# Performance work log

Hardware: AMD Instinct MI355X
Metric: run time of the kernel (lower is better)

## Reference

```python
import jax, jax.numpy as jnp
import numpy as np

DIM = 4096
N_HEADS = 32
N_KV_HEADS = 8
HEAD_DIM = 128
N_REP = N_HEADS // N_KV_HEADS  # 4
Q_DIM = N_HEADS * HEAD_DIM     # 4096
K_DIM = N_KV_HEADS * HEAD_DIM  # 1024
B, T = 2, 2048
ROPE_THETA = 10000.0


def setup_inputs() -> dict:
    key = jax.random.key(0)
    k1, k2, k3, k4 = jax.random.split(key, 4)
    x = jax.random.normal(k1, (B, T, DIM), dtype=jnp.float32)
    wqkv = jax.random.normal(k2, (Q_DIM + 2 * K_DIM, DIM), dtype=jnp.float32) * 0.02
    wo = jax.random.normal(k3, (DIM, DIM), dtype=jnp.float32) * 0.02
    # RoPE tables: [max_T, head_dim//2]
    inv_freq = 1.0 / (ROPE_THETA ** (jnp.arange(0, HEAD_DIM, 2, dtype=jnp.float32) / HEAD_DIM))
    angles = jnp.arange(T, dtype=jnp.float32)[:, None] * inv_freq[None, :]  # [T, D/2]
    cos = jnp.cos(angles)
    sin = jnp.sin(angles)
    freqs_cis = jax.random.normal(k4, (T, HEAD_DIM // 2), dtype=jnp.float32)  # unused by forward
    return {"x": x, "freqs_cis": freqs_cis, "wqkv": wqkv, "wo": wo, "cos": cos, "sin": sin}


def _apply_rope(q, k, cos, sin):
    # q: [B,T,Hq,D], k: [B,T,Hkv,D]; interleaved even/odd pairs
    Tlen = q.shape[1]
    c = cos[:Tlen][None, :, None, :]  # [1,T,1,D/2]
    s = sin[:Tlen][None, :, None, :]

    def rot(t):
        tr, ti = t[..., 0::2], t[..., 1::2]
        or_ = tr * c - ti * s
        oi = tr * s + ti * c
        return jnp.stack([or_, oi], axis=-1).reshape(t.shape)

    return rot(q), rot(k)


def reference(x, freqs_cis, wqkv, wo, cos, sin):
    Bx, Tx, _ = x.shape
    qkv = jnp.einsum('btd,ed->bte', x, wqkv)  # fused QKV GEMM
    q = qkv[..., :Q_DIM].reshape(Bx, Tx, N_HEADS, HEAD_DIM)
    k = qkv[..., Q_DIM:Q_DIM + K_DIM].reshape(Bx, Tx, N_KV_HEADS, HEAD_DIM)
    v = qkv[..., Q_DIM + K_DIM:].reshape(Bx, Tx, N_KV_HEADS, HEAD_DIM)
    q, k = _apply_rope(q, k, cos, sin)
    # GQA repeat_interleave over head dim
    k = jnp.repeat(k, N_REP, axis=2)  # [B,T,Hq,D]
    v = jnp.repeat(v, N_REP, axis=2)
    scale = 1.0 / jnp.sqrt(jnp.asarray(HEAD_DIM, dtype=q.dtype))
    scores = jnp.einsum('bqhd,bkhd->bhqk', q, k) * scale  # [B,H,T,T]
    causal = jnp.tril(jnp.ones((Tx, Tx), dtype=bool))
    scores = jnp.where(causal[None, None], scores, jnp.finfo(scores.dtype).min)
    probs = jax.nn.softmax(scores, axis=-1)
    y = jnp.einsum('bhqk,bkhd->bqhd', probs, v).reshape(Bx, Tx, Q_DIM)
    return jnp.einsum('btd,ed->bte', y, wo)
```

## Files before the change

kernel.cpp:

```cpp
#include <hip/hip_runtime.h>

#define T_SEQ 2048
#define NB    2
#define NH    32
#define NKV   8
#define HD    128
#define DIM   4096
#define EDIM  6144
#define M_TOK 4096

typedef __bf16          bf8  __attribute__((ext_vector_type(8)));
typedef unsigned short  us8  __attribute__((ext_vector_type(8)));
typedef float           f4   __attribute__((ext_vector_type(4)));
typedef float           f16v __attribute__((ext_vector_type(16)));
typedef int             i4   __attribute__((ext_vector_type(4)));

__device__ inline unsigned short f2bf(float f) {
  unsigned int u = __builtin_bit_cast(unsigned int, f);
  u += 0x7FFF + ((u >> 16) & 1);
  return (unsigned short)(u >> 16);
}
__device__ inline float bf2f(unsigned short h) {
  unsigned int u = ((unsigned int)h) << 16;
  return __builtin_bit_cast(float, u);
}
__device__ inline void gl_lds16(const void* g, void* l) {
  __builtin_amdgcn_global_load_lds(
      (const __attribute__((address_space(1))) unsigned int*)g,
      (__attribute__((address_space(3))) unsigned int*)l, 16, 0, 0);
}
__device__ inline f4 mfma16(bf8 a, bf8 b, f4 c) {
  return __builtin_amdgcn_mfma_f32_16x16x32_bf16(a, b, c, 0, 0, 0);
}
__device__ inline f16v mfma32(bf8 a, bf8 b, f16v c) {
  return __builtin_amdgcn_mfma_f32_32x32x16_bf16(a, b, c, 0, 0, 0);
}
__device__ inline unsigned cvtpk(float lo, float hi) {
  unsigned r;
  asm("v_cvt_pk_bf16_f32 %0, %1, %2" : "=v"(r) : "v"(lo), "v"(hi));
  return r;
}

__global__ void k_f2bf3(const float* __restrict__ x, const float* __restrict__ wq,
                        const float* __restrict__ wo,
                        unsigned short* __restrict__ xb, unsigned short* __restrict__ wqb,
                        unsigned short* __restrict__ wob) {
  const long n0 = (long)M_TOK * DIM / 4;
  const long n1 = (long)EDIM * DIM / 4;
  const long n2 = (long)DIM * DIM / 4;
  const long total = n0 + n1 + n2;
  const long stride = (long)gridDim.x * blockDim.x;
  for (long i = (long)blockIdx.x * blockDim.x + threadIdx.x; i < total; i += stride) {
    const float* in; unsigned short* out; long j = i;
    if (j < n0)              { in = x;  out = xb; }
    else if ((j -= n0) < n1) { in = wq; out = wqb; }
    else       { j -= n1;      in = wo; out = wob; }
    f4 v = *(const f4*)(in + j * 4);
    unsigned long long pack =
        (unsigned long long)f2bf(v[0]) |
        ((unsigned long long)f2bf(v[1]) << 16) |
        ((unsigned long long)f2bf(v[2]) << 32) |
        ((unsigned long long)f2bf(v[3]) << 48);
    *(unsigned long long*)(out + j * 4) = pack;
  }
}

__global__ __launch_bounds__(512, 2)
void k_gemm384(const unsigned short* __restrict__ A, const unsigned short* __restrict__ Bm,
               unsigned short* __restrict__ oQ, unsigned short* __restrict__ oK,
               unsigned short* __restrict__ oV) {
  __shared__ unsigned short As[2][8192];
  __shared__ unsigned short Bs[2][3][8192];
  const int n0 = blockIdx.x;
  const int x = n0 & 7, ix = n0 >> 3;
  const int bm = ((x >> 1) << 3) + (ix >> 3);
  const int bn = ((x & 1) << 3) + (ix & 7);
  const int t = threadIdx.x;
  const int lane = t & 63, w = t >> 6;
  const int wr = w >> 2, wc = w & 3;
  const int l15 = lane & 15, lhi = lane >> 4;
  const int KT = DIM >> 6;

  f4 acc[4][6] = {};

  const int tt0 = t * 8;
  auto stA = [&](int buf, int tile) {
    if (tile >= KT) return;
    const unsigned short* gp = A + (size_t)(bm * 128) * DIM + tile * 64;
#pragma unroll
    for (int j = 0; j < 2; ++j) {
      int e = j * 4096 + tt0;
      int rl = e >> 6, cs = (e & 63) ^ ((rl & 7) << 3);
      gl_lds16(gp + (size_t)rl * DIM + cs, &As[buf][e]);
    }
  };
  auto stB = [&](int buf, int bh, int tile) {
    if (tile >= KT) return;
    const unsigned short* gp = Bm + (size_t)(bn * 384 + bh * 128) * DIM + tile * 64;
#pragma unroll
    for (int j = 0; j < 2; ++j) {
      int e = j * 4096 + tt0;
      int rl = e >> 6, cs = (e & 63) ^ ((rl & 7) << 3);
      gl_lds16(gp + (size_t)rl * DIM + cs, &Bs[buf][bh][e]);
    }
  };
  auto rdA = [&](int buf, int mi, int kk) -> bf8 {
    int row = wr * 64 + mi * 16 + l15;
    int col = (lhi * 8 + kk * 32) ^ ((row & 7) << 3);
    return __builtin_bit_cast(bf8, *(const us8*)&As[buf][row * 64 + col]);
  };
  auto rdB = [&](int buf, int bh, int ni, int kk) -> bf8 {
    int row = wc * 32 + ni * 16 + l15;
    int col = (lhi * 8 + kk * 32) ^ ((row & 7) << 3);
    return __builtin_bit_cast(bf8, *(const us8*)&Bs[buf][bh][row * 64 + col]);
  };
  auto bar = [&]() {
    asm volatile("" ::: "memory");
    __builtin_amdgcn_s_barrier();
    asm volatile("" ::: "memory");
  };
  auto lgkm0 = [&]() {
    asm volatile("s_waitcnt lgkmcnt(0)" ::: "memory");
    __builtin_amdgcn_sched_barrier(0);
  };

  stA(0, 0); stB(0, 0, 0); stB(0, 1, 0); stB(0, 2, 0);
  asm volatile("s_waitcnt vmcnt(4)" ::: "memory");
  bar();

  for (int tp = 0; tp < KT; tp += 2) {
#pragma unroll
    for (int sub = 0; sub < 2; ++sub) {
      const int tc = tp + sub, b = sub;
      const bool last = (tc == KT - 1);
      bf8 af[4][2], bfr[2][2];
#pragma unroll
      for (int mi = 0; mi < 4; ++mi)
#pragma unroll
        for (int kk = 0; kk < 2; ++kk) af[mi][kk] = rdA(b, mi, kk);
#pragma unroll
      for (int ni = 0; ni < 2; ++ni)
#pragma unroll
        for (int kk = 0; kk < 2; ++kk) bfr[ni][kk] = rdB(b, 0, ni, kk);
      stA(b ^ 1, tc + 1); stB(b ^ 1, 0, tc + 1);
      lgkm0();
      __builtin_amdgcn_s_setprio(1);
#pragma unroll
      for (int mi = 0; mi < 4; ++mi)
#pragma unroll
        for (int ni = 0; ni < 2; ++ni)
#pragma unroll
          for (int kk = 0; kk < 2; ++kk)
            acc[mi][ni] = mfma16(af[mi][kk], bfr[ni][kk], acc[mi][ni]);
      __builtin_amdgcn_s_setprio(0);
      if (last) { asm volatile("s_waitcnt vmcnt(2)" ::: "memory"); }
      else      { asm volatile("s_waitcnt vmcnt(6)" ::: "memory"); }
      bar();
#pragma unroll
      for (int ni = 0; ni < 2; ++ni)
#pragma unroll
        for (int kk = 0; kk < 2; ++kk) bfr[ni][kk] = rdB(b, 1, ni, kk);
      stB(b ^ 1, 1, tc + 1);
      lgkm0();
      __builtin_amdgcn_s_setprio(1);
#pragma unroll
      for (int mi = 0; mi < 4; ++mi)
#pragma unroll
        for (int ni = 0; ni < 2; ++ni)
#pragma unroll
          for (int kk = 0; kk < 2; ++kk)
            acc[mi][2 + ni] = mfma16(af[mi][kk], bfr[ni][kk], acc[mi][2 + ni]);
      __builtin_amdgcn_s_setprio(0);
      if (last) { asm volatile("s_waitcnt vmcnt(0)" ::: "memory"); }
      else      { asm volatile("s_waitcnt vmcnt(6)" ::: "memory"); }
      bar();
#pragma unroll
      for (int ni = 0; ni < 2; ++ni)
#pragma unroll
        for (int kk = 0; kk < 2; ++kk) bfr[ni][kk] = rdB(b, 2, ni, kk);
      stB(b ^ 1, 2, tc + 1);
      lgkm0();
      __builtin_amdgcn_s_setprio(1);
#pragma unroll
      for (int mi = 0; mi < 4; ++mi)
#pragma unroll
        for (int ni = 0; ni < 2; ++ni)
#pragma unroll
          for (int kk = 0; kk < 2; ++kk)
            acc[mi][4 + ni] = mfma16(af[mi][kk], bfr[ni][kk], acc[mi][4 + ni]);
      __builtin_amdgcn_s_setprio(0);
      if (!last) { asm volatile("s_waitcnt vmcnt(4)" ::: "memory"); }
      bar();
    }
  }

#pragma unroll
  for (int bh = 0; bh < 3; ++bh)
#pragma unroll
    for (int ni = 0; ni < 2; ++ni) {
      const int colb = bn * 384 + bh * 128 + wc * 32 + ni * 16;
      unsigned short* op; int ldo, c0;
      if (colb < 4096)      { op = oQ; ldo = 4096; c0 = colb; }
      else if (colb < 5120) { op = oK; ldo = 1024; c0 = colb - 4096; }
      else                  { op = oV; ldo = 1024; c0 = colb - 5120; }
#pragma unroll
      for (int mi = 0; mi < 4; ++mi)
#pragma unroll
        for (int rr = 0; rr < 4; ++rr) {
          int row = bm * 128 + wr * 64 + mi * 16 + lhi * 4 + rr;
          op[(size_t)row * ldo + c0 + l15] = f2bf(acc[mi][bh * 2 + ni][rr]);
        }
    }
}

#define MFMA_Q(a0, b0, AF, BF)                                        \
  __builtin_amdgcn_s_setprio(1);                                      \
  _Pragma("unroll") for (int mi = 0; mi < 4; ++mi)                    \
  _Pragma("unroll") for (int ni = 0; ni < 2; ++ni)                    \
  _Pragma("unroll") for (int kk = 0; kk < 2; ++kk)                    \
      acc[(a0) + mi][(b0) + ni] =                                     \
          mfma16(AF[mi][kk], BF[ni][kk], acc[(a0) + mi][(b0) + ni]);  \
  __builtin_amdgcn_s_setprio(0);

#define RD_A(buf, mh)                                                 \
  _Pragma("unroll") for (int mi = 0; mi < 4; ++mi)                    \
  _Pragma("unroll") for (int kk = 0; kk < 2; ++kk)                    \
      af[mi][kk] = rdA(buf, mh, mi, kk);

#define RD_B(buf, nh, BF)                                             \
  _Pragma("unroll") for (int ni = 0; ni < 2; ++ni)                    \
  _Pragma("unroll") for (int kk = 0; kk < 2; ++kk)                    \
      BF[ni][kk] = rdB(buf, nh, ni, kk);

__global__ __launch_bounds__(512, 2)
void k_gemm256f(const unsigned short* __restrict__ A, const unsigned short* __restrict__ Bm,
                float* __restrict__ oF) {
  __shared__ unsigned short As[2][16384];
  __shared__ unsigned short Bs[2][16384];
  const int n0 = blockIdx.x;
  const int x = n0 & 7, ix = n0 >> 3;
  const int bm = ((x >> 1) << 2) + (ix >> 3);
  const int bn = ((x & 1) << 3) + (ix & 7);
  const int N = DIM, K = DIM;
  const int t = threadIdx.x;
  const int lane = t & 63, w = t >> 6;
  const int wr = w >> 2, wc = w & 3;
  const int l15 = lane & 15, lhi = lane >> 4;
  const int KT = K >> 6;
  const int NI = KT >> 1;

  f4 acc[8][4] = {};

  const int tt0 = t * 8;
  auto stA = [&](int buf, int half, int tile) {
    if (tile >= KT) return;
    const unsigned short* gp = A + (size_t)(bm * 256 + half * 128) * K + tile * 64;
#pragma unroll
    for (int j = 0; j < 2; ++j) {
      int e = j * 4096 + tt0;
      int rl = e >> 6;
      int cs = (e & 63) ^ ((rl & 7) << 3);
      gl_lds16(gp + (size_t)rl * K + cs, &As[buf][half * 8192 + e]);
    }
  };
  auto stB = [&](int buf, int half, int tile) {
    if (tile >= KT) return;
    const unsigned short* gp = Bm + (size_t)(bn * 256 + half * 128) * K + tile * 64;
#pragma unroll
    for (int j = 0; j < 2; ++j) {
      int e = j * 4096 + tt0;
      int rl = e >> 6;
      int cs = (e & 63) ^ ((rl & 7) << 3);
      gl_lds16(gp + (size_t)rl * K + cs, &Bs[buf][half * 8192 + e]);
    }
  };
  auto rdA = [&](int buf, int mh, int mi, int kk) -> bf8 {
    int row = mh * 128 + wr * 64 + mi * 16 + l15;
    int col = (lhi * 8 + kk * 32) ^ ((row & 7) << 3);
    return __builtin_bit_cast(bf8, *(const us8*)&As[buf][row * 64 + col]);
  };
  auto rdB = [&](int buf, int nh, int ni, int kk) -> bf8 {
    int row = nh * 128 + wc * 32 + ni * 16 + l15;
    int col = (lhi * 8 + kk * 32) ^ ((row & 7) << 3);
    return __builtin_bit_cast(bf8, *(const us8*)&Bs[buf][row * 64 + col]);
  };
  auto bar = [&]() {
    asm volatile("" ::: "memory");
    __builtin_amdgcn_s_barrier();
    asm volatile("" ::: "memory");
  };
  auto lgkm0 = [&]() {
    asm volatile("s_waitcnt lgkmcnt(0)" ::: "memory");
    __builtin_amdgcn_sched_barrier(0);
  };

  stA(0, 0, 0); stB(0, 1, 0); stA(0, 1, 0); stB(0, 0, 0);
  stA(1, 0, 1); stB(1, 1, 1); stA(1, 1, 1);
  asm volatile("s_waitcnt vmcnt(6)" ::: "memory");
  bar();

  for (int i = 0; i < NI; ++i) {
    const int t2 = 2 * i + 2, t3 = 2 * i + 3;
    bf8 af[4][2], bf0[2][2], bf1[2][2];
    RD_A(0, 0); RD_B(0, 0, bf0);
    stB(1, 0, 2 * i + 1);
    lgkm0();
    MFMA_Q(0, 0, af, bf0);
    bar();
    RD_B(0, 1, bf1);
    stA(0, 0, t2);
    lgkm0();
    MFMA_Q(0, 2, af, bf1);
    bar();
    RD_A(0, 1);
    stB(0, 1, t2);
    lgkm0();
    MFMA_Q(4, 2, af, bf1);
    bar();
    stA(0, 1, t2);
    MFMA_Q(4, 0, af, bf0);
    if (i + 1 < NI) { asm volatile("s_waitcnt vmcnt(6)" ::: "memory"); }
    else            { asm volatile("s_waitcnt vmcnt(0)" ::: "memory"); }
    bar();
    RD_A(1, 0); RD_B(1, 0, bf0);
    stB(0, 0, t2);
    lgkm0();
    MFMA_Q(0, 0, af, bf0);
    bar();
    RD_B(1, 1, bf1);
    stA(1, 0, t3);
    lgkm0();
    MFMA_Q(0, 2, af, bf1);
    bar();
    RD_A(1, 1);
    stB(1, 1, t3);
    lgkm0();
    MFMA_Q(4, 2, af, bf1);
    bar();
    stA(1, 1, t3);
    MFMA_Q(4, 0, af, bf0);
    if (i + 1 < NI) { asm volatile("s_waitcnt vmcnt(6)" ::: "memory"); }
    bar();
  }

  const int rb0 = bm * 256 + wr * 64 + lhi * 4;
  const int cb0 = bn * 256 + wc * 32 + l15;
#pragma unroll
  for (int ai = 0; ai < 8; ++ai)
#pragma unroll
    for (int bj = 0; bj < 4; ++bj)
#pragma unroll
      for (int rr = 0; rr < 4; ++rr) {
        int row = rb0 + (ai >> 2) * 128 + (ai & 3) * 16 + rr;
        int col = cb0 + (bj >> 1) * 128 + (bj & 1) * 16;
        oF[(size_t)row * N + col] = acc[ai][bj][rr];
      }
}

__global__ __launch_bounds__(512, 2)
void k_attn(const unsigned short* __restrict__ Qb, const unsigned short* __restrict__ Kb,
            const unsigned short* __restrict__ Vb, unsigned short* __restrict__ Yb,
            const float* __restrict__ cosp, const float* __restrict__ sinp) {
  __shared__ unsigned short Ks[64 * 128];
  __shared__ unsigned short Vt[128 * 64];
  const int idx = blockIdx.x;
  const int p = idx >> 6;
  const int hb = idx & 63;
  const int h = hb >> 1;
  const int b = hb & 1;
  const int kvh = h >> 2;
  const int t = threadIdx.x;
  const int lane = t & 63, w = t >> 6;
  const int l31 = lane & 31, hh = lane >> 5;
  const float BNEG = -1.0e30f;
  const float QSCALE = (float)(0.08838834764831845 * 1.4426950408889634);
  const int swz = (l31 & 7) << 3;
  const int krow = t >> 4;
  const int kcol = (t & 15) * 8;

  for (int qq = 0; qq < 2; ++qq) {
    const int qblk = qq ? p : 7 - p;
    const int qb0 = qblk * 256;
    const int NT = (qblk + 1) * 4;
    const int wqmin = qb0 + w * 32;
    const int q_g = wqmin + l31;

    bf8 qf[8];
    {
      const unsigned short* qp = Qb + (size_t)(b * T_SEQ + q_g) * 4096 + h * 128 + hh * 8;
#pragma unroll
      for (int st = 0; st < 8; ++st) {
        us8 v = *(const us8*)(qp + st * 16);
        f4 c = *(const f4*)(cosp + q_g * 64 + st * 8 + hh * 4);
        f4 s = *(const f4*)(sinp + q_g * 64 + st * 8 + hh * 4);
        us8 o;
#pragma unroll
        for (int j = 0; j < 4; ++j) {
          float tr = bf2f(v[2 * j]), ti = bf2f(v[2 * j + 1]);
          o[2 * j]     = f2bf((tr * c[j] - ti * s[j]) * QSCALE);
          o[2 * j + 1] = f2bf((tr * s[j] + ti * c[j]) * QSCALE);
        }
        qf[st] = __builtin_bit_cast(bf8, o);
      }
    }
    float m_run = BNEG, l_run = 0.f;
    f16v yacc[4] = {};

    for (int kt = 0; kt < NT; ++kt) {
      const int kbase = kt * 64;
      const unsigned short* vp = Vb + (size_t)(b * T_SEQ + kbase + lane) * 1024 + kvh * 128 + w * 8;
      us8 vv0 = *(const us8*)vp;
      us8 vv1 = *(const us8*)(vp + 64);
      const unsigned short* kp = Kb + (size_t)(b * T_SEQ + kbase + krow) * 1024 + kvh * 128 + kcol;
      us8 kk0 = *(const us8*)kp;
      us8 kk1 = *(const us8*)(kp + (size_t)32 * 1024);
      f4 kc0 = *(const f4*)(cosp + (kbase + krow) * 64 + (kcol >> 1));
      f4 ks0 = *(const f4*)(sinp + (kbase + krow) * 64 + (kcol >> 1));
      f4 kc1 = *(const f4*)(cosp + (kbase + krow + 32) * 64 + (kcol >> 1));
      f4 ks1 = *(const f4*)(sinp + (kbase + krow + 32) * 64 + (kcol >> 1));
      __syncthreads();
      {
        us8 o0, o1;
#pragma unroll
        for (int j = 0; j < 4; ++j) {
          float tr0 = bf2f(kk0[2 * j]), ti0 = bf2f(kk0[2 * j + 1]);
          o0[2 * j]     = f2bf(tr0 * kc0[j] - ti0 * ks0[j]);
          o0[2 * j + 1] = f2bf(tr0 * ks0[j] + ti0 * kc0[j]);
          float tr1 = bf2f(kk1[2 * j]), ti1 = bf2f(kk1[2 * j + 1]);
          o1[2 * j]     = f2bf(tr1 * kc1[j] - ti1 * ks1[j]);
          o1[2 * j + 1] = f2bf(tr1 * ks1[j] + ti1 * kc1[j]);
        }
        *(us8*)&Ks[krow * 128 + (kcol ^ ((krow & 7) << 3))] = o0;
        *(us8*)&Ks[(krow + 32) * 128 + (kcol ^ ((krow & 7) << 3))] = o1;
      }
#pragma unroll
      for (int j = 0; j < 8; ++j) {
        int d0 = w * 8 + j;
        Vt[(d0 * 64 + lane) ^ ((d0 & 7) << 3)] = vv0[j];
        int d1 = d0 + 64;
        Vt[(d1 * 64 + lane) ^ ((d1 & 7) << 3)] = vv1[j];
      }
      __syncthreads();
      if (kbase > wqmin + 31) continue;

      f16v s0 = {}, s1 = {};
#pragma unroll
      for (int st = 0; st < 8; ++st) {
        int coff = st * 16 + hh * 8;
        bf8 a0 = __builtin_bit_cast(bf8, *(const us8*)&Ks[(l31 * 128 + coff) ^ swz]);
        bf8 a1 = __builtin_bit_cast(bf8, *(const us8*)&Ks[((l31 + 32) * 128 + coff) ^ swz]);
        s0 = mfma32(a0, qf[st], s0);
        s1 = mfma32(a1, qf[st], s1);
      }
      if (kbase + 63 > wqmin) {
#pragma unroll
        for (int r = 0; r < 16; ++r) {
          int kv = kbase + (r & 3) + 8 * (r >> 2) + 4 * hh;
          if (kv > q_g)      s0[r] = BNEG;
          if (kv + 32 > q_g) s1[r] = BNEG;
        }
      }
      float tmax = BNEG;
#pragma unroll
      for (int r = 0; r < 16; ++r) {
        tmax = fmaxf(tmax, s0[r]);
        tmax = fmaxf(tmax, s1[r]);
      }
      tmax = fmaxf(tmax, __shfl_xor(tmax, 32));
      float m_new = fmaxf(m_run, tmax);
      float fac = exp2f(m_run - m_new);
      m_run = m_new;
      float psum = 0.f;
#pragma unroll
      for (int r = 0; r < 16; ++r) {
        s0[r] = exp2f(s0[r] - m_new); psum += s0[r];
        s1[r] = exp2f(s1[r] - m_new); psum += s1[r];
      }
      psum += __shfl_xor(psum, 32);
      l_run = l_run * fac + psum;
      if (!__all(fac == 1.0f)) {
        float facr[16];
#pragma unroll
        for (int r = 0; r < 16; ++r)
          facr[r] = __shfl(fac, (r & 3) + 8 * (r >> 2) + 4 * hh);
#pragma unroll
        for (int dc = 0; dc < 4; ++dc)
#pragma unroll
          for (int r = 0; r < 16; ++r) yacc[dc][r] *= facr[r];
      }
#pragma unroll
      for (int st = 0; st < 4; ++st) {
        f16v sv = (st & 2) ? s1 : s0;
        const int rb = (st & 1) * 8;
        unsigned pkA = cvtpk(sv[rb + 0], sv[rb + 1]);
        unsigned pkB = cvtpk(sv[rb + 2], sv[rb + 3]);
        unsigned pkC = cvtpk(sv[rb + 4], sv[rb + 5]);
        unsigned pkD = cvtpk(sv[rb + 6], sv[rb + 7]);
        unsigned xA = __shfl_xor(pkA, 32);
        unsigned xB = __shfl_xor(pkB, 32);
        unsigned xC = __shfl_xor(pkC, 32);
        unsigned xD = __shfl_xor(pkD, 32);
        unsigned w0 = hh ? xC : pkA;
        unsigned w1 = hh ? xD : pkB;
        unsigned w2 = hh ? pkC : xA;
        unsigned w3 = hh ? pkD : xB;
        i4 wi = { (int)w0, (int)w1, (int)w2, (int)w3 };
        bf8 pf = __builtin_bit_cast(bf8, wi);
#pragma unroll
        for (int dc = 0; dc < 4; ++dc) {
          int d = dc * 32 + l31;
          bf8 vf = __builtin_bit_cast(bf8, *(const us8*)&Vt[(d * 64 + st * 16 + hh * 8) ^ swz]);
          yacc[dc] = mfma32(pf, vf, yacc[dc]);
        }
      }
    }
    float inv_l = 1.0f / l_run;
    float il[16];
#pragma unroll
    for (int r = 0; r < 16; ++r)
      il[r] = __shfl(inv_l, (r & 3) + 8 * (r >> 2) + 4 * hh);
#pragma unroll
    for (int dc = 0; dc < 4; ++dc)
#pragma unroll
      for (int r = 0; r < 16; ++r) {
        int qrow = qb0 + w * 32 + (r & 3) + 8 * (r >> 2) + 4 * hh;
        Yb[(size_t)(b * T_SEQ + qrow) * 4096 + h * 128 + dc * 32 + l31] =
            f2bf(yacc[dc][r] * il[r]);
      }
  }
}

extern "C" void kernel_launch(void* const* d_in, const int* in_sizes, int n_in,
                              void* d_out, int out_size, void* d_ws, size_t ws_size,
                              hipStream_t stream) {
  const float* x    = (const float*)d_in[0];
  const float* wqkv = (const float*)d_in[2];
  const float* wo   = (const float*)d_in[3];
  const float* cosp = (const float*)d_in[4];
  const float* sinp = (const float*)d_in[5];
  float* out = (float*)d_out;

  char* ws = (char*)d_ws;
  size_t o = 0;
  auto alloc = [&](size_t bytes) { void* p = ws + o; o += (bytes + 255) & ~(size_t)255; return p; };
  unsigned short* x_b    = (unsigned short*)alloc((size_t)M_TOK * DIM * 2);
  unsigned short* wqkv_b = (unsigned short*)alloc((size_t)EDIM * DIM * 2);
  unsigned short* wo_b   = (unsigned short*)alloc((size_t)DIM * DIM * 2);
  unsigned short* Qb     = (unsigned short*)alloc((size_t)M_TOK * 4096 * 2);
  unsigned short* Kb     = (unsigned short*)alloc((size_t)M_TOK * 1024 * 2);
  unsigned short* Vb     = (unsigned short*)alloc((size_t)M_TOK * 1024 * 2);
  unsigned short* Yb     = (unsigned short*)alloc((size_t)M_TOK * 4096 * 2);
  if (o > ws_size) return;

  k_f2bf3<<<2048, 256, 0, stream>>>(x, wqkv, wo, x_b, wqkv_b, wo_b);

  k_gemm384<<<dim3(512), 512, 0, stream>>>(x_b, wqkv_b, Qb, Kb, Vb);

  k_attn<<<dim3(256, 1, 1), 512, 0, stream>>>(Qb, Kb, Vb, Yb, cosp, sinp);

  k_gemm256f<<<dim3(256), 512, 0, stream>>>(Yb, wo_b, out);
}
```

Before: 512.9 us.

## Single-buffer QKV GEMM LDS to raise occupancy to four blocks per CU

Replaces the double-buffered A/B LDS tiles (128KB) of the fused QKV GEMM with a single buffer (64KB) and raises the launch bound to four 512-thread blocks per CU. The loads for the next K tile are issued piecewise into sub-tiles as soon as each is consumed, with barriers and vmcnt waits reworked. This trades intra-block prefetch depth for more resident waves to hide latency. It risks exposing global load latency and register pressure from the tighter launch bound, which could spill the 24 accumulators.

```diff
diff --git a/kernel.cpp b/kernel.cpp
--- a/kernel.cpp
+++ b/kernel.cpp
@@ -65,12 +65,12 @@
   }
 }
 
-__global__ __launch_bounds__(512, 2)
+__global__ __launch_bounds__(512, 4)
 void k_gemm384(const unsigned short* __restrict__ A, const unsigned short* __restrict__ Bm,
                unsigned short* __restrict__ oQ, unsigned short* __restrict__ oK,
                unsigned short* __restrict__ oV) {
-  __shared__ unsigned short As[2][8192];
-  __shared__ unsigned short Bs[2][3][8192];
+  __shared__ unsigned short As[8192];
+  __shared__ unsigned short Bs[3][8192];
   const int n0 = blockIdx.x;
   const int x = n0 & 7, ix = n0 >> 3;
   const int bm = ((x >> 1) << 3) + (ix >> 3);
@@ -84,35 +84,35 @@
   f4 acc[4][6] = {};
 
   const int tt0 = t * 8;
-  auto stA = [&](int buf, int tile) {
+  auto stA = [&](int tile) {
     if (tile >= KT) return;
     const unsigned short* gp = A + (size_t)(bm * 128) * DIM + tile * 64;
 #pragma unroll
     for (int j = 0; j < 2; ++j) {
       int e = j * 4096 + tt0;
       int rl = e >> 6, cs = (e & 63) ^ ((rl & 7) << 3);
-      gl_lds16(gp + (size_t)rl * DIM + cs, &As[buf][e]);
-    }
-  };
-  auto stB = [&](int buf, int bh, int tile) {
+      gl_lds16(gp + (size_t)rl * DIM + cs, &As[e]);
+    }
+  };
+  auto stB = [&](int bh, int tile) {
     if (tile >= KT) return;
     const unsigned short* gp = Bm + (size_t)(bn * 384 + bh * 128) * DIM + tile * 64;
 #pragma unroll
     for (int j = 0; j < 2; ++j) {
       int e = j * 4096 + tt0;
       int rl = e >> 6, cs = (e & 63) ^ ((rl & 7) << 3);
-      gl_lds16(gp + (size_t)rl * DIM + cs, &Bs[buf][bh][e]);
-    }
-  };
-  auto rdA = [&](int buf, int mi, int kk) -> bf8 {
+      gl_lds16(gp + (size_t)rl * DIM + cs, &Bs[bh][e]);
+    }
+  };
+  auto rdA = [&](int mi, int kk) -> bf8 {
     int row = wr * 64 + mi * 16 + l15;
     int col = (lhi * 8 + kk * 32) ^ ((row & 7) << 3);
-    return __builtin_bit_cast(bf8, *(const us8*)&As[buf][row * 64 + col]);
-  };
-  auto rdB = [&](int buf, int bh, int ni, int kk) -> bf8 {
+    return __builtin_bit_cast(bf8, *(const us8*)&As[row * 64 + col]);
+  };
+  auto rdB = [&](int bh, int ni, int kk) -> bf8 {
     int row = wc * 32 + ni * 16 + l15;
     int col = (lhi * 8 + kk * 32) ^ ((row & 7) << 3);
-    return __builtin_bit_cast(bf8, *(const us8*)&Bs[buf][bh][row * 64 + col]);
+    return __builtin_bit_cast(bf8, *(const us8*)&Bs[bh][row * 64 + col]);
   };
   auto bar = [&]() {
     asm volatile("" ::: "memory");
@@ -124,72 +124,69 @@
     __builtin_amdgcn_sched_barrier(0);
   };
 
-  stA(0, 0); stB(0, 0, 0); stB(0, 1, 0); stB(0, 2, 0);
-  asm volatile("s_waitcnt vmcnt(4)" ::: "memory");
+  stA(0); stB(0, 0); stB(1, 0);
+  asm volatile("s_waitcnt vmcnt(2)" ::: "memory");
   bar();
 
-  for (int tp = 0; tp < KT; tp += 2) {
-#pragma unroll
-    for (int sub = 0; sub < 2; ++sub) {
-      const int tc = tp + sub, b = sub;
-      const bool last = (tc == KT - 1);
-      bf8 af[4][2], bfr[2][2];
-#pragma unroll
-      for (int mi = 0; mi < 4; ++mi)
-#pragma unroll
-        for (int kk = 0; kk < 2; ++kk) af[mi][kk] = rdA(b, mi, kk);
+  for (int tc = 0; tc < KT; ++tc) {
+    const bool last = (tc == KT - 1);
+    bf8 af[4][2], bfr[2][2];
+    stB(2, tc);
+#pragma unroll
+    for (int mi = 0; mi < 4; ++mi)
+#pragma unroll
+      for (int kk = 0; kk < 2; ++kk) af[mi][kk] = rdA(mi, kk);
+#pragma unroll
+    for (int ni = 0; ni < 2; ++ni)
+#pragma unroll
+      for (int kk = 0; kk < 2; ++kk) bfr[ni][kk] = rdB(0, ni, kk);
+    lgkm0();
+    __builtin_amdgcn_s_setprio(1);
+#pragma unroll
+    for (int mi = 0; mi < 4; ++mi)
 #pragma unroll
       for (int ni = 0; ni < 2; ++ni)
 #pragma unroll
-        for (int kk = 0; kk < 2; ++kk) bfr[ni][kk] = rdB(b, 0, ni, kk);
-      stA(b ^ 1, tc + 1); stB(b ^ 1, 0, tc + 1);
-      lgkm0();
-      __builtin_amdgcn_s_setprio(1);
-#pragma unroll
-      for (int mi = 0; mi < 4; ++mi)
-#pragma unroll
-        for (int ni = 0; ni < 2; ++ni)
-#pragma unroll
-          for (int kk = 0; kk < 2; ++kk)
-            acc[mi][ni] = mfma16(af[mi][kk], bfr[ni][kk], acc[mi][ni]);
-      __builtin_amdgcn_s_setprio(0);
-      if (last) { asm volatile("s_waitcnt vmcnt(2)" ::: "memory"); }
-      else      { asm volatile("s_waitcnt vmcnt(6)" ::: "memory"); }
-      bar();
+        for (int kk = 0; kk < 2; ++kk)
+          acc[mi][ni] = mfma16(af[mi][kk], bfr[ni][kk], acc[mi][ni]);
+    __builtin_amdgcn_s_setprio(0);
+    asm volatile("s_waitcnt vmcnt(2)" ::: "memory");
+    bar();
+    stA(tc + 1); stB(0, tc + 1);
+#pragma unroll
+    for (int ni = 0; ni < 2; ++ni)
+#pragma unroll
+      for (int kk = 0; kk < 2; ++kk) bfr[ni][kk] = rdB(1, ni, kk);
+    lgkm0();
+    __builtin_amdgcn_s_setprio(1);
+#pragma unroll
+    for (int mi = 0; mi < 4; ++mi)
 #pragma unroll
       for (int ni = 0; ni < 2; ++ni)
 #pragma unroll
-        for (int kk = 0; kk < 2; ++kk) bfr[ni][kk] = rdB(b, 1, ni, kk);
-      stB(b ^ 1, 1, tc + 1);
-      lgkm0();
-      __builtin_amdgcn_s_setprio(1);
-#pragma unroll
-      for (int mi = 0; mi < 4; ++mi)
-#pragma unroll
-        for (int ni = 0; ni < 2; ++ni)
-#pragma unroll
-          for (int kk = 0; kk < 2; ++kk)
-            acc[mi][2 + ni] = mfma16(af[mi][kk], bfr[ni][kk], acc[mi][2 + ni]);
-      __builtin_amdgcn_s_setprio(0);
-      if (last) { asm volatile("s_waitcnt vmcnt(0)" ::: "memory"); }
-      else      { asm volatile("s_waitcnt vmcnt(6)" ::: "memory"); }
-      bar();
+        for (int kk = 0; kk < 2; ++kk)
+          acc[mi][2 + ni] = mfma16(af[mi][kk], bfr[ni][kk], acc[mi][2 + ni]);
+    __builtin_amdgcn_s_setprio(0);
+    if (last) { asm volatile("s_waitcnt vmcnt(0)" ::: "memory"); }
+    else      { asm volatile("s_waitcnt vmcnt(4)" ::: "memory"); }
+    bar();
+    stB(1, tc + 1);
+#pragma unroll
+    for (int ni = 0; ni < 2; ++ni)
+#pragma unroll
+      for (int kk = 0; kk < 2; ++kk) bfr[ni][kk] = rdB(2, ni, kk);
+    lgkm0();
+    __builtin_amdgcn_s_setprio(1);
+#pragma unroll
+    for (int mi = 0; mi < 4; ++mi)
 #pragma unroll
       for (int ni = 0; ni < 2; ++ni)
 #pragma unroll
-        for (int kk = 0; kk < 2; ++kk) bfr[ni][kk] = rdB(b, 2, ni, kk);
-      stB(b ^ 1, 2, tc + 1);
-      lgkm0();
-      __builtin_amdgcn_s_setprio(1);
-#pragma unroll
-      for (int mi = 0; mi < 4; ++mi)
-#pragma unroll
-        for (int ni = 0; ni < 2; ++ni)
-#pragma unroll
-          for (int kk = 0; kk < 2; ++kk)
-            acc[mi][4 + ni] = mfma16(af[mi][kk], bfr[ni][kk], acc[mi][4 + ni]);
-      __builtin_amdgcn_s_setprio(0);
-      if (!last) { asm volatile("s_waitcnt vmcnt(4)" ::: "memory"); }
+        for (int kk = 0; kk < 2; ++kk)
+          acc[mi][4 + ni] = mfma16(af[mi][kk], bfr[ni][kk], acc[mi][4 + ni]);
+    __builtin_amdgcn_s_setprio(0);
+    if (!last) {
+      asm volatile("s_waitcnt vmcnt(2)" ::: "memory");
       bar();
     }
   }
```

After: 1.227 ms. +139.2%, slower.
